# Kernel optimization log

Hardware: AMD Instinct MI355X
Metric: run time of the kernel (lower is better)

## Reference

```python
import jax, jax.numpy as jnp
import numpy as np

NUM_HEADS = 12
EPS = 1e-6


def setup_inputs() -> dict:
    key = jax.random.key(0)
    k1, k2, k3, k4 = jax.random.split(key, 4)
    N, B, D = 1025, 8, 768
    x = jax.random.normal(k1, (N, B, D), dtype=jnp.float32)
    # torch nn.Linear weights: [out_features, in_features]
    w_qkv = jax.random.normal(k2, (3 * D, D), dtype=jnp.float32) * (D ** -0.5)
    w_proj = jax.random.normal(k3, (D, D), dtype=jnp.float32) * (D ** -0.5)
    b_proj = jax.random.normal(k4, (D,), dtype=jnp.float32) * 0.01
    return {"x": x, "w_qkv": w_qkv, "w_proj": w_proj, "b_proj": b_proj}


def reference(x, w_qkv, w_proj, b_proj):
    N, B, D = x.shape
    H = NUM_HEADS
    hd = D // H
    scale = hd ** -0.5
    scale_vv = scale * 1.0  # scale_multiplier = 1.0

    xb = jnp.transpose(x, (1, 0, 2))  # [B, N, D]
    qkv = xb @ w_qkv.T  # [B, N, 3D]
    qkv = qkv.reshape(B, N, 3, H, hd).transpose(2, 0, 3, 1, 4)  # [3, B, H, N, hd]
    q, k, v = qkv[0], qkv[1], qkv[2]

    # QK path: only row 0 of out_ori survives the masking, compute just that row
    scores0 = jnp.einsum('bhqd,bhkd->bhqk', q[:, :, :1], k) * scale  # [B,H,1,N]
    attn0 = jax.nn.softmax(scores0, axis=-1)
    out0 = jnp.einsum('bhqk,bhkd->bhqd', attn0, v)  # [B,H,1,hd]

    # VV cosine path: only rows 1: survive
    vn = v / jnp.maximum(jnp.linalg.norm(v, axis=-1, keepdims=True), EPS)
    scores_vv = jnp.einsum('bhqd,bhkd->bhqk', vn[:, :, 1:], vn) * scale_vv  # [B,H,N-1,N]
    attn_vv = jax.nn.softmax(scores_vv, axis=-1)
    out_vv = jnp.einsum('bhqk,bhkd->bhqd', attn_vv, v)  # [B,H,N-1,hd]

    out = jnp.concatenate([out0, out_vv], axis=2)  # [B,H,N,hd]
    out = out.transpose(0, 2, 1, 3).reshape(B, N, D)
    out = out @ w_proj.T + b_proj
    return jnp.transpose(out, (1, 0, 2))  # [N, B, D]
```

## Files before the change

kernel.cpp:

```cpp
#include <hip/hip_runtime.h>

typedef unsigned short u16;
typedef unsigned int   u32;
typedef __attribute__((ext_vector_type(8))) short short8;
typedef __attribute__((ext_vector_type(4))) float f32x4;

#define AS1 __attribute__((address_space(1)))
#define AS3 __attribute__((address_space(3)))

#define NSEQ  1025
#define BB    8
#define DD    768
#define HH    12
#define MROWS 8200
#define MPAD  8320
#define KPAD  1088

__device__ __forceinline__ void gl2lds16(const void* g, void* l) {
  __builtin_amdgcn_global_load_lds((const AS1 u32*)g, (AS3 u32*)l, 16, 0, 0);
}
__device__ __forceinline__ u16 f2bf(float f) {
  u32 u = __float_as_uint(f);
  return (u16)((u + 0x7FFFu + ((u >> 16) & 1u)) >> 16);
}
__device__ __forceinline__ float bf2f(u16 u) { return __uint_as_float(((u32)u) << 16); }

__global__ __launch_bounds__(256) void prep(const float* __restrict__ x,
                                            const float* __restrict__ wqkv,
                                            const float* __restrict__ wproj,
                                            u16* __restrict__ xb,
                                            u16* __restrict__ wkv,
                                            u16* __restrict__ wpj,
                                            float* __restrict__ q0) {
  __shared__ float red[256];
  const int XB_G  = MPAD * 192;
  const int WKV_G = 1536 * 192;
  int tid = threadIdx.x;
  if (blockIdx.x >= 7968) {
    int bid = blockIdx.x - 7968;
    int b = bid / HH, c = bid - b * HH;
    int dp = (c << 6) + (tid >> 2), part = tid & 3;
    const float4* x4 = (const float4*)(x + (size_t)b * DD + part * 192);
    const float4* w4 = (const float4*)(wqkv + (size_t)dp * DD + part * 192);
    float acc = 0.f;
#pragma unroll 4
    for (int e = 0; e < 48; ++e) {
      float4 a = x4[e], w = w4[e];
      acc += a.x * w.x + a.y * w.y + a.z * w.z + a.w * w.w;
    }
    red[tid] = acc;
    __syncthreads();
    if (part == 0) q0[b * DD + dp] = red[tid] + red[tid + 1] + red[tid + 2] + red[tid + 3];
    return;
  }
  int g = blockIdx.x * 256 + tid;
  float4 v;
  u16* dst;
  size_t di;
  if (g < XB_G) {
    int m = g / 192, e4 = g - m * 192;
    if (m < MROWS) {
      int bb = m / NSEQ, ns = m - bb * NSEQ;
      v = ((const float4*)x)[(size_t)(ns * BB + bb) * 192 + e4];
    } else {
      v.x = v.y = v.z = v.w = 0.f;
    }
    dst = xb; di = (size_t)g;
  } else if (g < XB_G + WKV_G) {
    int r = g - XB_G;
    v = ((const float4*)wqkv)[(size_t)147456 + r];
    dst = wkv; di = (size_t)r;
  } else {
    int r = g - XB_G - WKV_G;
    v = ((const float4*)wproj)[r];
    dst = wpj; di = (size_t)r;
  }
  uint2 o;
  o.x = (u32)f2bf(v.x) | ((u32)f2bf(v.y) << 16);
  o.y = (u32)f2bf(v.z) | ((u32)f2bf(v.w) << 16);
  ((uint2*)dst)[di] = o;
}

template <int MODE, int NT>
__global__ __launch_bounds__(256) void gemm_bt(const u16* __restrict__ A,
                                               const u16* __restrict__ W,
                                               u16* __restrict__ Cbf,
                                               float* __restrict__ Cf,
                                               const float* __restrict__ bias,
                                               int ldc) {
  __shared__ u16 sA[128 * 64];
  __shared__ u16 sW[128 * 64];
  const int id = blockIdx.x;
  const int rx = id & 7, qx = id >> 3;
  const int kq = qx / NT;
  const int m_t = rx + (kq << 3);
  if (m_t > 64) return;
  const int n_t = qx - kq * NT;
  const int m0 = m_t << 7, n0 = n_t << 7;

  const int tid = threadIdx.x;
  const int w = tid >> 6, lane = tid & 63;
  const int wm = w & 1, wn = w >> 1;
  const int lc = lane & 15, lr = lane >> 4;

  f32x4 zero4 = {0.f, 0.f, 0.f, 0.f};
  f32x4 acc[4][4];
#pragma unroll
  for (int i = 0; i < 4; ++i)
#pragma unroll
    for (int j = 0; j < 4; ++j) acc[i][j] = zero4;

  const int r0 = tid >> 3;
  const int ko = (tid & 7) << 3;
  const u16* gA = A + (size_t)(m0 + r0) * DD + ko;
  const u16* gW = W + (size_t)(n0 + r0) * DD + ko;
  char* lA = (char*)sA + tid * 16;
  char* lW = (char*)sW + tid * 16;

#pragma unroll 1
  for (int kt = 0; kt < 12; ++kt) {
    __syncthreads();
#pragma unroll
    for (int j = 0; j < 4; ++j) {
      gl2lds16(gA + (size_t)j * 32 * DD + kt * 64, lA + j * 4096);
      gl2lds16(gW + (size_t)j * 32 * DD + kt * 64, lW + j * 4096);
    }
    __syncthreads();
#pragma unroll
    for (int kk = 0; kk < 2; ++kk) {
      short8 af[4], wf[4];
#pragma unroll
      for (int mt = 0; mt < 4; ++mt)
        af[mt] = *(const short8*)((char*)sA + ((wm << 6) + (mt << 4) + lc) * 128 + (kk << 6) + (lr << 4));
#pragma unroll
      for (int nt = 0; nt < 4; ++nt)
        wf[nt] = *(const short8*)((char*)sW + ((wn << 6) + (nt << 4) + lc) * 128 + (kk << 6) + (lr << 4));
#pragma unroll
      for (int mt = 0; mt < 4; ++mt)
#pragma unroll
        for (int nt = 0; nt < 4; ++nt)
          acc[mt][nt] = __builtin_amdgcn_mfma_f32_16x16x32_bf16(af[mt], wf[nt], acc[mt][nt], 0, 0, 0);
    }
  }

  if (MODE == 0) {
#pragma unroll
    for (int mt = 0; mt < 4; ++mt)
#pragma unroll
      for (int r = 0; r < 4; ++r) {
        int m = m0 + (wm << 6) + (mt << 4) + (lr << 2) + r;
        if (m < MROWS) {
          size_t base = (size_t)m * ldc + n0 + (wn << 6) + lc;
#pragma unroll
          for (int nt = 0; nt < 4; ++nt) Cbf[base + (nt << 4)] = f2bf(acc[mt][nt][r]);
        }
      }
  } else {
    float b4[4];
#pragma unroll
    for (int nt = 0; nt < 4; ++nt) b4[nt] = bias[n0 + (wn << 6) + (nt << 4) + lc];
#pragma unroll
    for (int mt = 0; mt < 4; ++mt)
#pragma unroll
      for (int r = 0; r < 4; ++r) {
        int m = m0 + (wm << 6) + (mt << 4) + (lr << 2) + r;
        if (m < MROWS) {
          int bb = m / NSEQ;
          int ns = m - bb * NSEQ;
          float* o = Cf + (size_t)ns * (BB * DD) + bb * DD + n0 + (wn << 6) + lc;
#pragma unroll
          for (int nt = 0; nt < 4; ++nt) o[nt << 4] = acc[mt][nt][r] + b4[nt];
        }
      }
  }
}

__global__ __launch_bounds__(256) void transpose_v(const u16* __restrict__ kv,
                                                   u16* __restrict__ vT,
                                                   u16* __restrict__ vn) {
  __shared__ u16 tile[64][72];
  __shared__ float red[256];
  __shared__ float sInv[64];
  int bid = blockIdx.x;
  int kc = bid % 17;
  int t2 = bid / 17;
  int h = t2 % HH, b = t2 / HH;
  int tid = threadIdx.x;
  int kl = tid >> 2, dc = (tid & 3) << 4;
  int key = kc * 64 + kl;
  u32 vals[8];
  if (key < NSEQ) {
    const u32* g = (const u32*)(kv + ((size_t)b * NSEQ + key) * 1536 + DD + h * 64 + dc);
#pragma unroll
    for (int i = 0; i < 8; ++i) vals[i] = g[i];
  } else {
#pragma unroll
    for (int i = 0; i < 8; ++i) vals[i] = 0;
  }
  float part = 0.f;
#pragma unroll
  for (int i = 0; i < 8; ++i) {
    float a = bf2f((u16)(vals[i] & 0xFFFF));
    float c = bf2f((u16)(vals[i] >> 16));
    part += a * a + c * c;
    ((u32*)&tile[kl][dc])[i] = vals[i];
  }
  red[tid] = part;
  __syncthreads();
  if ((tid & 3) == 0) {
    float s = red[tid] + red[tid + 1] + red[tid + 2] + red[tid + 3];
    sInv[kl] = (key < NSEQ) ? 1.0f / fmaxf(sqrtf(s), 1e-6f) : 0.0f;
  }
  __syncthreads();
  float iv = sInv[kl];
  u32 ovn[8];
#pragma unroll
  for (int i = 0; i < 8; ++i) {
    float a = bf2f((u16)(vals[i] & 0xFFFF)) * iv;
    float c = bf2f((u16)(vals[i] >> 16)) * iv;
    ovn[i] = (u32)f2bf(a) | ((u32)f2bf(c) << 16);
  }
  u32* on = (u32*)(vn + ((size_t)(b * HH + h) * KPAD + key) * 64 + dc);
#pragma unroll
  for (int i = 0; i < 8; ++i) on[i] = ovn[i];
  int dl = tid >> 2, ks = (tid & 3) << 4;
  u32 ov[8];
#pragma unroll
  for (int i = 0; i < 8; ++i)
    ov[i] = (u32)tile[ks + 2 * i][dl] | ((u32)tile[ks + 2 * i + 1][dl] << 16);
  u16* o = vT + (size_t)(b * HH + h) * 64 * KPAD + (size_t)dl * KPAD + kc * 64 + ks;
#pragma unroll
  for (int i = 0; i < 8; ++i) ((u32*)o)[i] = ov[i];
}

__global__ __launch_bounds__(256) void row0_attn(const float* __restrict__ q0,
                                                 const u16* __restrict__ kv,
                                                 u16* __restrict__ attn) {
  __shared__ float sq[64];
  __shared__ float sc[NSEQ];
  __shared__ float red[256];
  __shared__ float rpv[32][68];
  int bid = blockIdx.x;
  int b = bid / HH, h = bid - b * HH;
  int tid = threadIdx.x;
  if (tid < 64) sq[tid] = q0[b * DD + h * 64 + tid];
  __syncthreads();
  float mx = -1e30f;
  for (int n = tid; n < NSEQ; n += 256) {
    const u32* kr = (const u32*)(kv + ((size_t)b * NSEQ + n) * 1536 + h * 64);
    float s = 0.f;
#pragma unroll
    for (int i = 0; i < 32; ++i) {
      u32 u = kr[i];
      s += bf2f((u16)(u & 0xFFFF)) * sq[2 * i] + bf2f((u16)(u >> 16)) * sq[2 * i + 1];
    }
    s *= 0.125f;
    sc[n] = s;
    mx = fmaxf(mx, s);
  }
  red[tid] = mx;
  __syncthreads();
  for (int st = 128; st > 0; st >>= 1) {
    if (tid < st) red[tid] = fmaxf(red[tid], red[tid + st]);
    __syncthreads();
  }
  mx = red[0];
  __syncthreads();
  float ds = 0.f;
  for (int n = tid; n < NSEQ; n += 256) {
    float p = __expf(sc[n] - mx);
    sc[n] = p;
    ds += p;
  }
  red[tid] = ds;
  __syncthreads();
  for (int st = 128; st > 0; st >>= 1) {
    if (tid < st) red[tid] += red[tid + st];
    __syncthreads();
  }
  float den = red[0];
  __syncthreads();
  int kp = tid >> 3, dc = (tid & 7) << 3;
  const u16* vb = kv + (size_t)b * NSEQ * 1536 + DD + h * 64 + dc;
  float acc[8];
#pragma unroll
  for (int i = 0; i < 8; ++i) acc[i] = 0.f;
#pragma unroll 4
  for (int j = 0; j < 32; ++j) {
    int n = kp + (j << 5);
    uint4 v = *(const uint4*)(vb + (size_t)n * 1536);
    float p = sc[n];
    acc[0] += p * bf2f((u16)(v.x & 0xFFFF));
    acc[1] += p * bf2f((u16)(v.x >> 16));
    acc[2] += p * bf2f((u16)(v.y & 0xFFFF));
    acc[3] += p * bf2f((u16)(v.y >> 16));
    acc[4] += p * bf2f((u16)(v.z & 0xFFFF));
    acc[5] += p * bf2f((u16)(v.z >> 16));
    acc[6] += p * bf2f((u16)(v.w & 0xFFFF));
    acc[7] += p * bf2f((u16)(v.w >> 16));
  }
  if (kp == 0) {
    uint4 v = *(const uint4*)(vb + (size_t)1024 * 1536);
    float p = sc[1024];
    acc[0] += p * bf2f((u16)(v.x & 0xFFFF));
    acc[1] += p * bf2f((u16)(v.x >> 16));
    acc[2] += p * bf2f((u16)(v.y & 0xFFFF));
    acc[3] += p * bf2f((u16)(v.y >> 16));
    acc[4] += p * bf2f((u16)(v.z & 0xFFFF));
    acc[5] += p * bf2f((u16)(v.z >> 16));
    acc[6] += p * bf2f((u16)(v.w & 0xFFFF));
    acc[7] += p * bf2f((u16)(v.w >> 16));
  }
#pragma unroll
  for (int i = 0; i < 8; ++i) rpv[kp][dc + i] = acc[i];
  __syncthreads();
  if (tid < 64) {
    float s = 0.f;
#pragma unroll
    for (int p = 0; p < 32; ++p) s += rpv[p][tid];
    attn[(size_t)b * NSEQ * DD + h * 64 + tid] = f2bf(s / den);
  }
}

__global__ __launch_bounds__(256) void vv_attn(const u16* __restrict__ vn,
                                               const u16* __restrict__ vT,
                                               u16* __restrict__ attn) {
  __shared__ u16 sQ[2 * 128 * 32];
  __shared__ u16 sK[2 * 64 * 32];
  __shared__ u16 sV[2 * 64 * 32];
  __shared__ u16 sP[128 * 72];

  const int tid = threadIdx.x, w = tid >> 6, lane = tid & 63;
  const int lc = lane & 15, lr = lane >> 4;
  const int bh = blockIdx.x;
  const int m0 = blockIdx.y << 7;
  const int b = bh / HH, h = bh - b * HH;
  const char* nb = (const char*)(vn + (size_t)bh * KPAD * 64);
  const char* tb = (const char*)(vT + (size_t)bh * 64 * KPAD);

#pragma unroll
  for (int j = 0; j < 4; ++j) {
    int lin = (w << 12) + (j << 10) + (lane << 4);
    int hf = lin >> 13, r = (lin >> 6) & 127, off = lin & 63;
    gl2lds16(nb + (size_t)(1 + m0 + r) * 128 + hf * 64 + off, (char*)sQ + lin);
  }

  f32x4 zero4 = {0.f, 0.f, 0.f, 0.f};
  f32x4 oacc[2][4];
  f32x4 dacc[2];
#pragma unroll
  for (int i = 0; i < 2; ++i) {
    dacc[i] = zero4;
#pragma unroll
    for (int j = 0; j < 4; ++j) oacc[i][j] = zero4;
  }
  short8 ones;
#pragma unroll
  for (int i = 0; i < 8; ++i) ones[i] = (short)0x3F80;

  const float CEXP = 0.1803368801111204f;

#pragma unroll 1
  for (int kt = 0; kt < 17; ++kt) {
    __syncthreads();
#pragma unroll
    for (int j = 0; j < 2; ++j) {
      int lin = (w << 11) + (j << 10) + (lane << 4);
      int hf = lin >> 12, r = (lin >> 6) & 63, off = lin & 63;
      gl2lds16(nb + (size_t)(kt * 64 + r) * 128 + hf * 64 + off, (char*)sK + lin);
      gl2lds16(tb + (size_t)r * (KPAD * 2) + kt * 128 + hf * 64 + off, (char*)sV + lin);
    }
    __syncthreads();

    f32x4 sacc[4][2];
#pragma unroll
    for (int mt = 0; mt < 4; ++mt)
#pragma unroll
      for (int nt = 0; nt < 2; ++nt) sacc[mt][nt] = zero4;
#pragma unroll
    for (int kk = 0; kk < 2; ++kk) {
      short8 ak[4], bq[2];
#pragma unroll
      for (int mt = 0; mt < 4; ++mt)
        ak[mt] = *(const short8*)((char*)sK + (kk << 12) + ((mt << 4) + lc) * 64 + (lr << 4));
#pragma unroll
      for (int nt = 0; nt < 2; ++nt)
        bq[nt] = *(const short8*)((char*)sQ + (kk << 13) + ((w << 5) + (nt << 4) + lc) * 64 + (lr << 4));
#pragma unroll
      for (int mt = 0; mt < 4; ++mt)
#pragma unroll
        for (int nt = 0; nt < 2; ++nt)
          sacc[mt][nt] = __builtin_amdgcn_mfma_f32_16x16x32_bf16(ak[mt], bq[nt], sacc[mt][nt], 0, 0, 0);
    }

#pragma unroll
    for (int mt = 0; mt < 4; ++mt) {
      int kl0 = (mt << 4) + (lr << 2);
#pragma unroll
      for (int nt = 0; nt < 2; ++nt) {
        int q = (w << 5) + (nt << 4) + lc;
        u32 a0 = __float_as_uint(__builtin_amdgcn_exp2f(sacc[mt][nt][0] * CEXP)) + 0x8000u;
        u32 a1 = __float_as_uint(__builtin_amdgcn_exp2f(sacc[mt][nt][1] * CEXP)) + 0x8000u;
        u32 a2 = __float_as_uint(__builtin_amdgcn_exp2f(sacc[mt][nt][2] * CEXP)) + 0x8000u;
        u32 a3 = __float_as_uint(__builtin_amdgcn_exp2f(sacc[mt][nt][3] * CEXP)) + 0x8000u;
        uint2 pv;
        pv.x = __builtin_amdgcn_perm(a1, a0, 0x07060302u);
        pv.y = __builtin_amdgcn_perm(a3, a2, 0x07060302u);
        if (kt == 16) {
          pv.x = (kl0 == 0) ? (pv.x & 0xFFFFu) : 0u;
          pv.y = 0u;
        }
        *(uint2*)((char*)sP + q * 144 + (kl0 << 1)) = pv;
      }
    }

#pragma unroll
    for (int kk = 0; kk < 2; ++kk) {
      short8 ap[2], bv[4];
#pragma unroll
      for (int mt = 0; mt < 2; ++mt)
        ap[mt] = *(const short8*)((char*)sP + ((w << 5) + (mt << 4) + lc) * 144 + (kk << 6) + (lr << 4));
#pragma unroll
      for (int nt = 0; nt < 4; ++nt)
        bv[nt] = *(const short8*)((char*)sV + (kk << 12) + ((nt << 4) + lc) * 64 + (lr << 4));
#pragma unroll
      for (int mt = 0; mt < 2; ++mt) {
#pragma unroll
        for (int nt = 0; nt < 4; ++nt)
          oacc[mt][nt] = __builtin_amdgcn_mfma_f32_16x16x32_bf16(ap[mt], bv[nt], oacc[mt][nt], 0, 0, 0);
        dacc[mt] = __builtin_amdgcn_mfma_f32_16x16x32_bf16(ap[mt], ones, dacc[mt], 0, 0, 0);
      }
    }
  }

#pragma unroll
  for (int mt = 0; mt < 2; ++mt) {
#pragma unroll
    for (int r = 0; r < 4; ++r) {
      int q = (w << 5) + (mt << 4) + (lr << 2) + r;
      int nseq = 1 + m0 + q;
      float rdn = 1.0f / dacc[mt][r];
      size_t obase = ((size_t)b * NSEQ + nseq) * DD + h * 64 + lc;
#pragma unroll
      for (int nt = 0; nt < 4; ++nt) attn[obase + (nt << 4)] = f2bf(oacc[mt][nt][r] * rdn);
    }
  }
}

extern "C" void kernel_launch(void* const* d_in, const int* in_sizes, int n_in,
                              void* d_out, int out_size, void* d_ws, size_t ws_size,
                              hipStream_t stream) {
  const float* x      = (const float*)d_in[0];
  const float* w_qkv  = (const float*)d_in[1];
  const float* w_proj = (const float*)d_in[2];
  const float* b_proj = (const float*)d_in[3];
  float* out = (float*)d_out;
  char* ws = (char*)d_ws;

  u16*   xb   = (u16*)(ws + 0);
  u16*   vT   = (u16*)(ws + 0);
  u16*   wkv  = (u16*)(ws + 13369344);
  u16*   wpj  = (u16*)(ws + 15728640);
  u16*   kvb  = (u16*)(ws + 16908288);
  float* q0   = (float*)(ws + 42467328);
  u16*   attn = (u16*)(ws + 42491904);
  u16*   vn   = (u16*)(ws + 55271424);

  prep<<<8064, 256, 0, stream>>>(x, w_qkv, w_proj, xb, wkv, wpj, q0);
  gemm_bt<0, 12><<<864, 256, 0, stream>>>(xb, wkv, kvb, nullptr, nullptr, 1536);
  transpose_v<<<1632, 256, 0, stream>>>(kvb, vT, vn);
  row0_attn<<<96, 256, 0, stream>>>(q0, kvb, attn);
  vv_attn<<<dim3(96, 8), 256, 0, stream>>>(vn, vT, attn);
  gemm_bt<1, 6><<<432, 256, 0, stream>>>(attn, wpj, nullptr, out, b_proj, 768);
}
```

Before: 239.2 us.

## Drop K projection by folding q0 into Wk and fuse row0 into V transpose

The row-0 attention scores are now computed as x·(Wk^T q0), so the K half of the QKV GEMM is no longer produced. This halves the first GEMM and the prep conversion work. The row-0 attention kernel is merged into the V transpose/normalise kernel as extra blocks, which removes one launch. The softmax exponent scale is folded into the V normalisation constant so the vv_attn inner loop skips a multiply. In exchange, the row-0 path reads fp32 x and Wk directly with per-block matvecs, and the folded scale changes where rounding happens.

Measured after the change: 316.5 us. 1.32x slower.

```diff
diff --git a/kernel.cpp b/kernel.cpp
--- a/kernel.cpp
+++ b/kernel.cpp
@@ -29,15 +29,15 @@
                                             const float* __restrict__ wqkv,
                                             const float* __restrict__ wproj,
                                             u16* __restrict__ xb,
-                                            u16* __restrict__ wkv,
+                                            u16* __restrict__ wv,
                                             u16* __restrict__ wpj,
                                             float* __restrict__ q0) {
   __shared__ float red[256];
-  const int XB_G  = MPAD * 192;
-  const int WKV_G = 1536 * 192;
+  const int XB_G = MPAD * 192;
+  const int WV_G = 768 * 192;
   int tid = threadIdx.x;
-  if (blockIdx.x >= 7968) {
-    int bid = blockIdx.x - 7968;
+  if (blockIdx.x >= 7392) {
+    int bid = blockIdx.x - 7392;
     int b = bid / HH, c = bid - b * HH;
     int dp = (c << 6) + (tid >> 2), part = tid & 3;
     const float4* x4 = (const float4*)(x + (size_t)b * DD + part * 192);
@@ -66,12 +66,12 @@
       v.x = v.y = v.z = v.w = 0.f;
     }
     dst = xb; di = (size_t)g;
-  } else if (g < XB_G + WKV_G) {
+  } else if (g < XB_G + WV_G) {
     int r = g - XB_G;
-    v = ((const float4*)wqkv)[(size_t)147456 + r];
-    dst = wkv; di = (size_t)r;
+    v = ((const float4*)wqkv)[(size_t)294912 + r];
+    dst = wv; di = (size_t)r;
   } else {
-    int r = g - XB_G - WKV_G;
+    int r = g - XB_G - WV_G;
     v = ((const float4*)wproj)[r];
     dst = wpj; di = (size_t)r;
   }
@@ -175,22 +175,130 @@
   }
 }
 
-__global__ __launch_bounds__(256) void transpose_v(const u16* __restrict__ kv,
-                                                   u16* __restrict__ vT,
-                                                   u16* __restrict__ vn) {
+__global__ __launch_bounds__(256) void tv_row0(const u16* __restrict__ vb,
+                                               u16* __restrict__ vT,
+                                               u16* __restrict__ vn,
+                                               const float* __restrict__ x,
+                                               const float* __restrict__ wqkv,
+                                               const float* __restrict__ q0,
+                                               u16* __restrict__ attn) {
+  __shared__ float red[256];
+  int tid = threadIdx.x;
+  if (blockIdx.x >= 1632) {
+    __shared__ float sq[64];
+    __shared__ float st[768];
+    __shared__ float sc[NSEQ];
+    __shared__ float rpv[32][68];
+    int bid2 = blockIdx.x - 1632;
+    int b = bid2 / HH, h = bid2 - b * HH;
+    if (tid < 64) sq[tid] = q0[b * DD + h * 64 + tid];
+    __syncthreads();
+    {
+      float t0 = 0.f, t1 = 0.f, t2 = 0.f;
+      const float* wk = wqkv + (size_t)(768 + h * 64) * DD;
+#pragma unroll 4
+      for (int d = 0; d < 64; ++d) {
+        float qd = sq[d];
+        const float* wr = wk + (size_t)d * DD;
+        t0 += qd * wr[tid];
+        t1 += qd * wr[tid + 256];
+        t2 += qd * wr[tid + 512];
+      }
+      st[tid] = t0; st[tid + 256] = t1; st[tid + 512] = t2;
+    }
+    __syncthreads();
+    float mx = -1e30f;
+    const float4* st4 = (const float4*)st;
+    for (int j = 0; j < 5; ++j) {
+      int n = tid + (j << 8);
+      if (n > 1024) break;
+      const float4* xr = (const float4*)(x + ((size_t)n * BB + b) * DD);
+      float s = 0.f;
+#pragma unroll 8
+      for (int c = 0; c < 192; ++c) {
+        float4 a = xr[c], t = st4[c];
+        s += a.x * t.x + a.y * t.y + a.z * t.z + a.w * t.w;
+      }
+      s *= 0.125f;
+      sc[n] = s;
+      mx = fmaxf(mx, s);
+    }
+    red[tid] = mx;
+    __syncthreads();
+    for (int stp = 128; stp > 0; stp >>= 1) {
+      if (tid < stp) red[tid] = fmaxf(red[tid], red[tid + stp]);
+      __syncthreads();
+    }
+    mx = red[0];
+    __syncthreads();
+    float ds = 0.f;
+    for (int n = tid; n < NSEQ; n += 256) {
+      float p = __expf(sc[n] - mx);
+      sc[n] = p;
+      ds += p;
+    }
+    red[tid] = ds;
+    __syncthreads();
+    for (int stp = 128; stp > 0; stp >>= 1) {
+      if (tid < stp) red[tid] += red[tid + stp];
+      __syncthreads();
+    }
+    float den = red[0];
+    __syncthreads();
+    int kp = tid >> 3, dc = (tid & 7) << 3;
+    const u16* vp = vb + ((size_t)b * NSEQ) * DD + h * 64 + dc;
+    float acc[8];
+#pragma unroll
+    for (int i = 0; i < 8; ++i) acc[i] = 0.f;
+#pragma unroll 4
+    for (int j = 0; j < 32; ++j) {
+      int n = kp + (j << 5);
+      uint4 v = *(const uint4*)(vp + (size_t)n * DD);
+      float p = sc[n];
+      acc[0] += p * bf2f((u16)(v.x & 0xFFFF));
+      acc[1] += p * bf2f((u16)(v.x >> 16));
+      acc[2] += p * bf2f((u16)(v.y & 0xFFFF));
+      acc[3] += p * bf2f((u16)(v.y >> 16));
+      acc[4] += p * bf2f((u16)(v.z & 0xFFFF));
+      acc[5] += p * bf2f((u16)(v.z >> 16));
+      acc[6] += p * bf2f((u16)(v.w & 0xFFFF));
+      acc[7] += p * bf2f((u16)(v.w >> 16));
+    }
+    if (kp == 0) {
+      uint4 v = *(const uint4*)(vp + (size_t)1024 * DD);
+      float p = sc[1024];
+      acc[0] += p * bf2f((u16)(v.x & 0xFFFF));
+      acc[1] += p * bf2f((u16)(v.x >> 16));
+      acc[2] += p * bf2f((u16)(v.y & 0xFFFF));
+      acc[3] += p * bf2f((u16)(v.y >> 16));
+      acc[4] += p * bf2f((u16)(v.z & 0xFFFF));
+      acc[5] += p * bf2f((u16)(v.z >> 16));
+      acc[6] += p * bf2f((u16)(v.w & 0xFFFF));
+      acc[7] += p * bf2f((u16)(v.w >> 16));
+    }
+#pragma unroll
+    for (int i = 0; i < 8; ++i) rpv[kp][dc + i] = acc[i];
+    __syncthreads();
+    if (tid < 64) {
+      float s = 0.f;
+#pragma unroll
+      for (int p = 0; p < 32; ++p) s += rpv[p][tid];
+      attn[(size_t)b * NSEQ * DD + h * 64 + tid] = f2bf(s / den);
+    }
+    return;
+  }
+
   __shared__ u16 tile[64][72];
-  __shared__ float red[256];
   __shared__ float sInv[64];
   int bid = blockIdx.x;
   int kc = bid % 17;
   int t2 = bid / 17;
   int h = t2 % HH, b = t2 / HH;
-  int tid = threadIdx.x;
   int kl = tid >> 2, dc = (tid & 3) << 4;
   int key = kc * 64 + kl;
   u32 vals[8];
   if (key < NSEQ) {
-    const u32* g = (const u32*)(kv + ((size_t)b * NSEQ + key) * 1536 + DD + h * 64 + dc);
+    const u32* g = (const u32*)(vb + ((size_t)b * NSEQ + key) * DD + h * 64 + dc);
 #pragma unroll
     for (int i = 0; i < 8; ++i) vals[i] = g[i];
   } else {
@@ -209,7 +317,7 @@
   __syncthreads();
   if ((tid & 3) == 0) {
     float s = red[tid] + red[tid + 1] + red[tid + 2] + red[tid + 3];
-    sInv[kl] = (key < NSEQ) ? 1.0f / fmaxf(sqrtf(s), 1e-6f) : 0.0f;
+    sInv[kl] = (key < NSEQ) ? 0.42466088f / fmaxf(sqrtf(s), 1e-6f) : 0.0f;
   }
   __syncthreads();
   float iv = sInv[kl];
@@ -231,95 +339,6 @@
   u16* o = vT + (size_t)(b * HH + h) * 64 * KPAD + (size_t)dl * KPAD + kc * 64 + ks;
 #pragma unroll
   for (int i = 0; i < 8; ++i) ((u32*)o)[i] = ov[i];
-}
-
-__global__ __launch_bounds__(256) void row0_attn(const float* __restrict__ q0,
-                                                 const u16* __restrict__ kv,
-                                                 u16* __restrict__ attn) {
-  __shared__ float sq[64];
-  __shared__ float sc[NSEQ];
-  __shared__ float red[256];
-  __shared__ float rpv[32][68];
-  int bid = blockIdx.x;
-  int b = bid / HH, h = bid - b * HH;
-  int tid = threadIdx.x;
-  if (tid < 64) sq[tid] = q0[b * DD + h * 64 + tid];
-  __syncthreads();
-  float mx = -1e30f;
-  for (int n = tid; n < NSEQ; n += 256) {
-    const u32* kr = (const u32*)(kv + ((size_t)b * NSEQ + n) * 1536 + h * 64);
-    float s = 0.f;
-#pragma unroll
-    for (int i = 0; i < 32; ++i) {
-      u32 u = kr[i];
-      s += bf2f((u16)(u & 0xFFFF)) * sq[2 * i] + bf2f((u16)(u >> 16)) * sq[2 * i + 1];
-    }
-    s *= 0.125f;
-    sc[n] = s;
-    mx = fmaxf(mx, s);
-  }
-  red[tid] = mx;
-  __syncthreads();
-  for (int st = 128; st > 0; st >>= 1) {
-    if (tid < st) red[tid] = fmaxf(red[tid], red[tid + st]);
-    __syncthreads();
-  }
-  mx = red[0];
-  __syncthreads();
-  float ds = 0.f;
-  for (int n = tid; n < NSEQ; n += 256) {
-    float p = __expf(sc[n] - mx);
-    sc[n] = p;
-    ds += p;
-  }
-  red[tid] = ds;
-  __syncthreads();
-  for (int st = 128; st > 0; st >>= 1) {
-    if (tid < st) red[tid] += red[tid + st];
-    __syncthreads();
-  }
-  float den = red[0];
-  __syncthreads();
-  int kp = tid >> 3, dc = (tid & 7) << 3;
-  const u16* vb = kv + (size_t)b * NSEQ * 1536 + DD + h * 64 + dc;
-  float acc[8];
-#pragma unroll
-  for (int i = 0; i < 8; ++i) acc[i] = 0.f;
-#pragma unroll 4
-  for (int j = 0; j < 32; ++j) {
-    int n = kp + (j << 5);
-    uint4 v = *(const uint4*)(vb + (size_t)n * 1536);
-    float p = sc[n];
-    acc[0] += p * bf2f((u16)(v.x & 0xFFFF));
-    acc[1] += p * bf2f((u16)(v.x >> 16));
-    acc[2] += p * bf2f((u16)(v.y & 0xFFFF));
-    acc[3] += p * bf2f((u16)(v.y >> 16));
-    acc[4] += p * bf2f((u16)(v.z & 0xFFFF));
-    acc[5] += p * bf2f((u16)(v.z >> 16));
-    acc[6] += p * bf2f((u16)(v.w & 0xFFFF));
-    acc[7] += p * bf2f((u16)(v.w >> 16));
-  }
-  if (kp == 0) {
-    uint4 v = *(const uint4*)(vb + (size_t)1024 * 1536);
-    float p = sc[1024];
-    acc[0] += p * bf2f((u16)(v.x & 0xFFFF));
-    acc[1] += p * bf2f((u16)(v.x >> 16));
-    acc[2] += p * bf2f((u16)(v.y & 0xFFFF));
-    acc[3] += p * bf2f((u16)(v.y >> 16));
-    acc[4] += p * bf2f((u16)(v.z & 0xFFFF));
-    acc[5] += p * bf2f((u16)(v.z >> 16));
-    acc[6] += p * bf2f((u16)(v.w & 0xFFFF));
-    acc[7] += p * bf2f((u16)(v.w >> 16));
-  }
-#pragma unroll
-  for (int i = 0; i < 8; ++i) rpv[kp][dc + i] = acc[i];
-  __syncthreads();
-  if (tid < 64) {
-    float s = 0.f;
-#pragma unroll
-    for (int p = 0; p < 32; ++p) s += rpv[p][tid];
-    attn[(size_t)b * NSEQ * DD + h * 64 + tid] = f2bf(s / den);
-  }
 }
 
 __global__ __launch_bounds__(256) void vv_attn(const u16* __restrict__ vn,
@@ -358,8 +377,6 @@
 #pragma unroll
   for (int i = 0; i < 8; ++i) ones[i] = (short)0x3F80;
 
-  const float CEXP = 0.1803368801111204f;
-
 #pragma unroll 1
   for (int kt = 0; kt < 17; ++kt) {
     __syncthreads();
@@ -399,10 +416,10 @@
 #pragma unroll
       for (int nt = 0; nt < 2; ++nt) {
         int q = (w << 5) + (nt << 4) + lc;
-        u32 a0 = __float_as_uint(__builtin_amdgcn_exp2f(sacc[mt][nt][0] * CEXP)) + 0x8000u;
-        u32 a1 = __float_as_uint(__builtin_amdgcn_exp2f(sacc[mt][nt][1] * CEXP)) + 0x8000u;
-        u32 a2 = __float_as_uint(__builtin_amdgcn_exp2f(sacc[mt][nt][2] * CEXP)) + 0x8000u;
-        u32 a3 = __float_as_uint(__builtin_amdgcn_exp2f(sacc[mt][nt][3] * CEXP)) + 0x8000u;
+        u32 a0 = __float_as_uint(__builtin_amdgcn_exp2f(sacc[mt][nt][0])) + 0x8000u;
+        u32 a1 = __float_as_uint(__builtin_amdgcn_exp2f(sacc[mt][nt][1])) + 0x8000u;
+        u32 a2 = __float_as_uint(__builtin_amdgcn_exp2f(sacc[mt][nt][2])) + 0x8000u;
+        u32 a3 = __float_as_uint(__builtin_amdgcn_exp2f(sacc[mt][nt][3])) + 0x8000u;
         uint2 pv;
         pv.x = __builtin_amdgcn_perm(a1, a0, 0x07060302u);
         pv.y = __builtin_amdgcn_perm(a3, a2, 0x07060302u);
@@ -459,17 +476,16 @@
 
   u16*   xb   = (u16*)(ws + 0);
   u16*   vT   = (u16*)(ws + 0);
-  u16*   wkv  = (u16*)(ws + 13369344);
-  u16*   wpj  = (u16*)(ws + 15728640);
-  u16*   kvb  = (u16*)(ws + 16908288);
-  float* q0   = (float*)(ws + 42467328);
-  u16*   attn = (u16*)(ws + 42491904);
-  u16*   vn   = (u16*)(ws + 55271424);
-
-  prep<<<8064, 256, 0, stream>>>(x, w_qkv, w_proj, xb, wkv, wpj, q0);
-  gemm_bt<0, 12><<<864, 256, 0, stream>>>(xb, wkv, kvb, nullptr, nullptr, 1536);
-  transpose_v<<<1632, 256, 0, stream>>>(kvb, vT, vn);
-  row0_attn<<<96, 256, 0, stream>>>(q0, kvb, attn);
+  u16*   wv   = (u16*)(ws + 13369344);
+  u16*   wpj  = (u16*)(ws + 14548992);
+  u16*   vb   = (u16*)(ws + 15728640);
+  float* q0   = (float*)(ws + 28508160);
+  u16*   attn = (u16*)(ws + 28532736);
+  u16*   vn   = (u16*)(ws + 41312256);
+
+  prep<<<7488, 256, 0, stream>>>(x, w_qkv, w_proj, xb, wv, wpj, q0);
+  gemm_bt<0, 6><<<432, 256, 0, stream>>>(xb, wv, vb, nullptr, nullptr, 768);
+  tv_row0<<<1728, 256, 0, stream>>>(vb, vT, vn, x, w_qkv, q0, attn);
   vv_attn<<<dim3(96, 8), 256, 0, stream>>>(vn, vT, attn);
   gemm_bt<1, 6><<<432, 256, 0, stream>>>(attn, wpj, nullptr, out, b_proj, 768);
 }
```
